# Kernel optimization log

Measured on AMD Instinct MI355X. Metric: run time of the kernel, lower is better.

## Reference

```python
import jax, jax.numpy as jnp
import numpy as np

NUM_HEADS = 4
NUM_GROUPS = 8
EPS = 1e-5


def setup_inputs() -> dict:
    key = jax.random.key(0)
    ks = jax.random.split(key, 4)
    b, c, h, w = 16, 512, 32, 32
    x = jax.random.normal(ks[0], (b, c, h, w), dtype=jnp.float32)
    gamma = jnp.ones((c,), dtype=jnp.float32)
    beta = jnp.zeros((c,), dtype=jnp.float32)
    # conv1d kernel-size-1 weights expressed as [out, in] matrices
    w_qkv = jax.random.normal(ks[1], (3 * c, c), dtype=jnp.float32) * (1.0 / np.sqrt(c))
    b_qkv = jnp.zeros((3 * c,), dtype=jnp.float32)
    w_proj = jax.random.normal(ks[2], (c, c), dtype=jnp.float32) * (1.0 / np.sqrt(c))
    b_proj = jnp.zeros((c,), dtype=jnp.float32)
    return {"x": x, "gamma": gamma, "beta": beta, "w_qkv": w_qkv,
            "b_qkv": b_qkv, "w_proj": w_proj, "b_proj": b_proj}


def group_norm(x, gamma, beta):
    # x: [b, c, h, w]; normalize per (group) over (c/g, h, w)
    b, c, h, w = x.shape
    xg = x.reshape(b, NUM_GROUPS, c // NUM_GROUPS, h, w)
    mean = xg.mean(axis=(2, 3, 4), keepdims=True)
    var = xg.var(axis=(2, 3, 4), keepdims=True)
    xn = ((xg - mean) * jax.lax.rsqrt(var + EPS)).reshape(b, c, h, w)
    return xn * gamma[None, :, None, None] + beta[None, :, None, None]


def reference(x, gamma, beta, w_qkv, b_qkv, w_proj, b_proj):
    b, c, h, w = x.shape
    L = h * w
    hd = c // NUM_HEADS  # head_dim
    x_in = x
    xn = group_norm(x, gamma, beta).reshape(b, c, L)
    # 1x1 conv == matmul over channel dim: [b, 3c, L]
    qkv = jnp.einsum('oc,bcl->bol', w_qkv, xn) + b_qkv[None, :, None]
    q, k, v = jnp.split(qkv, 3, axis=1)  # each [b, c, L]
    q = q.reshape(b, NUM_HEADS, hd, L)
    k = k.reshape(b, NUM_HEADS, hd, L)
    v = v.reshape(b, NUM_HEADS, hd, L)
    scale = hd ** (-0.5)
    attn = jnp.einsum('bhdl,bhdm->bhlm', q * scale, k)  # [b,h,L,L]
    attn = jax.nn.softmax(attn, axis=-1)
    out = jnp.einsum('bhlm,bhdm->bhdl', attn, v).reshape(b, c, L)
    out = jnp.einsum('oc,bcl->bol', w_proj, out) + b_proj[None, :, None]
    return x_in + out.reshape(b, c, h, w)
```

## Files before the change

### kernel.cpp

```cpp
#include <hip/hip_runtime.h>
#include <hip/hip_bf16.h>

typedef __hip_bfloat16 bf16;
typedef __attribute__((ext_vector_type(8))) short short8;
typedef __attribute__((ext_vector_type(4))) float f32x4;
typedef __attribute__((ext_vector_type(16))) float f32x16;

__device__ __forceinline__ float b2f(bf16 v) { return __bfloat162float(v); }
__device__ __forceinline__ bf16  f2b(float v) { return __float2bfloat16(v); }

__device__ __forceinline__ unsigned cvt_pk_bf16(float lo, float hi) {
    unsigned r;
    asm("v_cvt_pk_bf16_f32 %0, %1, %2" : "=v"(r) : "v"(lo), "v"(hi));
    return r;
}

__global__ __launch_bounds__(256) void pre_kernel(
    const float* __restrict__ wq, const float* __restrict__ wp,
    bf16* __restrict__ wqb, bf16* __restrict__ wpb,
    const float* __restrict__ x,
    float* __restrict__ partS, float* __restrict__ partQ)
{
    const int bid = blockIdx.x;
    const int t = threadIdx.x;
    if (bid < 1024) {
        int ch = bid * 256 + t;
        float4 v;
        bf16* dst;
        if (ch < 196608) {
            v = ((const float4*)wq)[ch];
            dst = wqb + ch * 4;
        } else {
            int c2 = ch - 196608;
            v = ((const float4*)wp)[c2];
            dst = wpb + c2 * 4;
        }
        bf16 o[4] = {f2b(v.x), f2b(v.y), f2b(v.z), f2b(v.w)};
        *(uint2*)dst = *(const uint2*)o;
        return;
    }
    const int pb = bid - 1024;
    const size_t base = (size_t)pb * 16384;

    float sum = 0.f, ssq = 0.f;
    const float4* x4 = (const float4*)(x + base);
    for (int i = t; i < 4096; i += 256) {
        float4 v = x4[i];
        sum += v.x + v.y + v.z + v.w;
        ssq += v.x * v.x + v.y * v.y + v.z * v.z + v.w * v.w;
    }
    #pragma unroll
    for (int off = 32; off > 0; off >>= 1) {
        sum += __shfl_down(sum, off);
        ssq += __shfl_down(ssq, off);
    }
    __shared__ float red[8];
    const int wid = t >> 6, lane = t & 63;
    if (lane == 0) { red[wid] = sum; red[4 + wid] = ssq; }
    __syncthreads();
    if (t == 0) {
        partS[pb] = red[0] + red[1] + red[2] + red[3];
        partQ[pb] = red[4] + red[5] + red[6] + red[7];
    }
}

__global__ __launch_bounds__(256) void gn_apply_t_kernel(
    const float* __restrict__ x,
    const float* __restrict__ partS, const float* __restrict__ partQ,
    const float* __restrict__ gamma, const float* __restrict__ beta,
    bf16* __restrict__ Xt)
{
    const int lt = blockIdx.x, ct = blockIdx.y, b = blockIdx.z;
    const int l0 = lt * 64, c0 = ct * 64;
    const int t = threadIdx.x;
    __shared__ float Ls[64][65];

    const int bg = b * 8 + ct;
    float s = partS[bg * 4] + partS[bg * 4 + 1] + partS[bg * 4 + 2] + partS[bg * 4 + 3];
    float q = partQ[bg * 4] + partQ[bg * 4 + 1] + partQ[bg * 4 + 2] + partQ[bg * 4 + 3];
    float mean = s * (1.f / 65536.f);
    float var  = q * (1.f / 65536.f) - mean * mean;
    float rstd = rsqrtf(var + 1e-5f);

    const float* xb = x + ((size_t)b * 512 + c0) * 1024 + l0;
    for (int i = t; i < 1024; i += 256) {
        int cc = i >> 4, lc = (i & 15) * 4;
        float4 v = *(const float4*)(xb + (size_t)cc * 1024 + lc);
        float sc = rstd * gamma[c0 + cc];
        float sh = beta[c0 + cc] - mean * sc;
        Ls[cc][lc]     = v.x * sc + sh;
        Ls[cc][lc + 1] = v.y * sc + sh;
        Ls[cc][lc + 2] = v.z * sc + sh;
        Ls[cc][lc + 3] = v.w * sc + sh;
    }
    __syncthreads();
    for (int i = t; i < 1024; i += 256) {
        int l = i >> 4, cc = (i & 15) * 4;
        bf16 o[4] = {f2b(Ls[cc][l]), f2b(Ls[cc + 1][l]),
                     f2b(Ls[cc + 2][l]), f2b(Ls[cc + 3][l])};
        *(uint2*)(Xt + ((size_t)b * 1024 + l0 + l) * 512 + c0 + cc) = *(const uint2*)o;
    }
}

__global__ __launch_bounds__(256) void mfma_qkv_kernel(
    const bf16* __restrict__ W,
    const bf16* __restrict__ Xt,
    const float* __restrict__ bias,
    bf16* __restrict__ Qt,
    bf16* __restrict__ Kt,
    bf16* __restrict__ Vb)
{
    const int n0 = blockIdx.x * 128;
    const int m0 = blockIdx.y * 128;
    const int b  = blockIdx.z;
    const int t  = threadIdx.x;
    const int w  = t >> 6, lane = t & 63;
    const int c  = lane & 15, quad = lane >> 4;
    const int w0 = w & 1, w1 = w >> 1;
    const int ak = quad * 8;

    __shared__ __align__(16) bf16 smem[18432];
    bf16* As = smem;
    bf16* Bs = smem + 9216;
    bf16* Cs = smem;

    const bf16* Ag = W + (size_t)m0 * 512;
    const bf16* Bg = Xt + ((size_t)b * 1024 + n0) * 512;

    const int srow = t >> 3, skc = (t & 7) * 8;

    short8 areg[4], breg[4];
    #pragma unroll
    for (int p = 0; p < 4; p++) {
        int row = srow + p * 32;
        areg[p] = *(const short8*)(Ag + (size_t)row * 512 + skc);
        breg[p] = *(const short8*)(Bg + (size_t)row * 512 + skc);
    }

    f32x4 acc[4][4];
    #pragma unroll
    for (int i = 0; i < 4; i++)
        #pragma unroll
        for (int j = 0; j < 4; j++)
            #pragma unroll
            for (int r = 0; r < 4; r++) acc[i][j][r] = 0.f;

    for (int k0 = 0; k0 < 512; k0 += 64) {
        __syncthreads();
        #pragma unroll
        for (int p = 0; p < 4; p++) {
            int row = srow + p * 32;
            *(short8*)&As[row * 72 + skc] = areg[p];
            *(short8*)&Bs[row * 72 + skc] = breg[p];
        }
        __syncthreads();
        {
            int k1 = (k0 + 64) & 511;
            #pragma unroll
            for (int p = 0; p < 4; p++) {
                int row = srow + p * 32;
                areg[p] = *(const short8*)(Ag + (size_t)row * 512 + k1 + skc);
                breg[p] = *(const short8*)(Bg + (size_t)row * 512 + k1 + skc);
            }
        }
        #pragma unroll
        for (int kk = 0; kk < 2; kk++) {
            short8 af[4], bf[4];
            #pragma unroll
            for (int jm = 0; jm < 4; jm++)
                af[jm] = *(const short8*)&As[(w0 * 64 + jm * 16 + c) * 72 + kk * 32 + ak];
            #pragma unroll
            for (int jn = 0; jn < 4; jn++)
                bf[jn] = *(const short8*)&Bs[(w1 * 64 + jn * 16 + c) * 72 + kk * 32 + ak];
            #pragma unroll
            for (int jm = 0; jm < 4; jm++)
                #pragma unroll
                for (int jn = 0; jn < 4; jn++)
                    acc[jm][jn] = __builtin_amdgcn_mfma_f32_16x16x32_bf16(
                        af[jm], bf[jn], acc[jm][jn], 0, 0, 0);
        }
    }

    __syncthreads();
    const int cls = m0 >> 9;
    if (cls < 2) {
        #pragma unroll
        for (int jm = 0; jm < 4; jm++) {
            #pragma unroll
            for (int jn = 0; jn < 4; jn++) {
                bf16 o4[4];
                #pragma unroll
                for (int r = 0; r < 4; r++) {
                    int orow = w0 * 64 + jm * 16 + quad * 4 + r;
                    o4[r] = f2b(acc[jm][jn][r] + bias[m0 + orow]);
                }
                *(uint2*)&Cs[(size_t)(w1 * 64 + jn * 16 + c) * 136
                             + w0 * 64 + jm * 16 + quad * 4] = *(const uint2*)o4;
            }
        }
        __syncthreads();
        const int head = (m0 >> 7) & 3;
        bf16* Db = (cls == 0 ? Qt : Kt)
                   + (((size_t)(b * 4 + head)) * 1024 + n0) * 128;
        for (int i = t; i < 2048; i += 256) {
            int row = i >> 4, ch = (i & 15) * 8;
            *(short8*)(Db + (size_t)row * 128 + ch) = *(const short8*)&Cs[row * 136 + ch];
        }
    } else {
        #pragma unroll
        for (int jm = 0; jm < 4; jm++) {
            #pragma unroll
            for (int r = 0; r < 4; r++) {
                int orow = w0 * 64 + jm * 16 + quad * 4 + r;
                float bs = bias[m0 + orow];
                #pragma unroll
                for (int jn = 0; jn < 4; jn++)
                    Cs[orow * 136 + w1 * 64 + jn * 16 + c] = f2b(acc[jm][jn][r] + bs);
            }
        }
        __syncthreads();
        bf16* Cb = Vb + ((size_t)b * 512 + (m0 - 1024)) * 1024 + n0;
        for (int i = t; i < 2048; i += 256) {
            int row = i >> 4, ch = (i & 15) * 8;
            *(short8*)(Cb + (size_t)row * 1024 + ch) = *(const short8*)&Cs[row * 136 + ch];
        }
    }
}

#define HD 128
#define QT 256
#define MT 64

__global__ __launch_bounds__(512, 2) void attn_mfma_kernel(
    const bf16* __restrict__ Qt,
    const bf16* __restrict__ Kt,
    const bf16* __restrict__ Vb,
    bf16* __restrict__ out)
{
    const int bh = blockIdx.x;
    const int qt = blockIdx.y;
    const int b = bh >> 2, h = bh & 3;
    const int t = threadIdx.x;
    const int w = t >> 6, lane = t & 63;
    const int wrow = lane & 31;
    const int blk  = lane >> 5;
    const int l0 = qt * QT;

    __shared__ __align__(16) bf16 smem[34816];

    const int qrow = w * 32 + wrow;
    const bf16* Qr = Qt + (((size_t)(b * 4 + h)) * 1024 + l0 + qrow) * 128;
    short8 aq[8];
    #pragma unroll
    for (int kt = 0; kt < 8; kt++)
        aq[kt] = *(const short8*)(Qr + kt * 16 + blk * 8);

    const bf16* Kb = Kt + (((size_t)(b * 4 + h)) * 1024) * 128;
    const bf16* Vg = Vb + ((size_t)(b * 512 + h * HD)) * 1024;

    bf16* Ks = smem;
    bf16* Vs = smem + 8704;

    short8 kreg[2], vreg[2];
    #pragma unroll
    for (int p = 0; p < 2; p++) {
        int i = t + p * 512;
        kreg[p] = *(const short8*)(Kb + (size_t)(i >> 4) * 128 + (i & 15) * 8);
        vreg[p] = *(const short8*)(Vg + (size_t)(i >> 3) * 1024 + (i & 7) * 8);
    }

    f32x16 acc_o[4];
    #pragma unroll
    for (int n = 0; n < 4; n++)
        #pragma unroll
        for (int r = 0; r < 16; r++) acc_o[n][r] = 0.f;

    float psl4[4] = {0.f, 0.f, 0.f, 0.f};

    const float kSc = 0.08838834764831845f * 1.4426950408889634f;
    const float kSh = 6.0f * 1.4426950408889634f;

    for (int mt = 0; mt < 1024 / MT; mt++) {
        __syncthreads();
        #pragma unroll
        for (int p = 0; p < 2; p++) {
            int i = t + p * 512;
            int m = i >> 4;
            int mrow = (m & 51) | ((m & 4) << 1) | ((m & 8) >> 1);
            *(short8*)&Ks[mrow * 136 + (i & 15) * 8] = kreg[p];
            *(short8*)&Vs[(i >> 3) * 72 + (i & 7) * 8]  = vreg[p];
        }
        __syncthreads();

        {
            int m0n = (mt < 15) ? (mt + 1) * MT : 0;
            #pragma unroll
            for (int p = 0; p < 2; p++) {
                int i = t + p * 512;
                kreg[p] = *(const short8*)(Kb + (size_t)(m0n + (i >> 4)) * 128 + (i & 15) * 8);
                vreg[p] = *(const short8*)(Vg + (size_t)(i >> 3) * 1024 + m0n + (i & 7) * 8);
            }
        }

        f32x16 accs[2];
        #pragma unroll
        for (int n = 0; n < 2; n++)
            #pragma unroll
            for (int r = 0; r < 16; r++) accs[n][r] = 0.f;
        __builtin_amdgcn_s_setprio(1);
        #pragma unroll
        for (int kt = 0; kt < 8; kt++) {
            #pragma unroll
            for (int nt = 0; nt < 2; nt++) {
                short8 afr = *(const short8*)&Ks[(nt * 32 + wrow) * 136 + kt * 16 + blk * 8];
                accs[nt] = __builtin_amdgcn_mfma_f32_32x32x16_bf16(afr, aq[kt], accs[nt], 0, 0, 0);
            }
        }
        __builtin_amdgcn_s_setprio(0);

        unsigned pw[2][8];
        #pragma unroll
        for (int nt = 0; nt < 2; nt++) {
            float pv[16];
            #pragma unroll
            for (int r = 0; r < 16; r++)
                pv[r] = exp2f(accs[nt][r] * kSc - kSh);
            #pragma unroll
            for (int r = 0; r < 16; r++) psl4[r & 3] += pv[r];
            #pragma unroll
            for (int wd = 0; wd < 8; wd++)
                pw[nt][wd] = cvt_pk_bf16(pv[2 * wd], pv[2 * wd + 1]);
        }

        __builtin_amdgcn_s_setprio(1);
        #pragma unroll
        for (int kt2 = 0; kt2 < 4; kt2++) {
            union { short8 s; unsigned u[4]; } pa;
            #pragma unroll
            for (int wd = 0; wd < 4; wd++)
                pa.u[wd] = pw[kt2 >> 1][(kt2 & 1) * 4 + wd];
            #pragma unroll
            for (int nt2 = 0; nt2 < 4; nt2++) {
                short8 bv = *(const short8*)&Vs[(nt2 * 32 + wrow) * 72 + kt2 * 16 + blk * 8];
                acc_o[nt2] = __builtin_amdgcn_mfma_f32_32x32x16_bf16(pa.s, bv, acc_o[nt2], 0, 0, 0);
            }
        }
        __builtin_amdgcn_s_setprio(0);
    }

    float psl = (psl4[0] + psl4[1]) + (psl4[2] + psl4[3]);
    float tot = psl + __shfl_xor(psl, 32);
    float inv[16];
    #pragma unroll
    for (int r = 0; r < 16; r++) {
        int q = (r & 3) + 8 * (r >> 2) + 4 * blk;
        inv[r] = __builtin_amdgcn_rcpf(__shfl(tot, q | (lane & 32)));
    }

    __syncthreads();
    bf16* Os = smem;
    #pragma unroll
    for (int nt2 = 0; nt2 < 4; nt2++)
        #pragma unroll
        for (int r = 0; r < 16; r++) {
            int row = w * 32 + (r & 3) + 8 * (r >> 2) + 4 * blk;
            Os[row * 136 + nt2 * 32 + wrow] = f2b(acc_o[nt2][r] * inv[r]);
        }
    __syncthreads();
    bf16* Ob = out + ((size_t)b * 1024 + l0) * 512 + h * HD;
    for (int i = t; i < 4096; i += 512) {
        int row = i >> 4, ch = (i & 15) * 8;
        *(short8*)(Ob + (size_t)row * 512 + ch) = *(const short8*)&Os[row * 136 + ch];
    }
}

__global__ __launch_bounds__(256) void mfma_proj_kernel(
    const bf16* __restrict__ W,
    const bf16* __restrict__ Xt,
    const float* __restrict__ bias,
    const float* __restrict__ res,
    float* __restrict__ C)
{
    const int n0 = blockIdx.x * 128;
    const int m0 = blockIdx.y * 128;
    const int b  = blockIdx.z;
    const int t  = threadIdx.x;
    const int w  = t >> 6, lane = t & 63;
    const int c  = lane & 15, quad = lane >> 4;
    const int w0 = w & 1, w1 = w >> 1;
    const int ak = quad * 8;

    __shared__ __align__(16) bf16 smem[18432];
    bf16* As = smem;
    bf16* Bs = smem + 9216;
    bf16* Cs = smem;

    const bf16* Ag = W + (size_t)m0 * 512;
    const bf16* Bg = Xt + ((size_t)b * 1024 + n0) * 512;

    const int srow = t >> 3, skc = (t & 7) * 8;

    short8 areg[4], breg[4];
    #pragma unroll
    for (int p = 0; p < 4; p++) {
        int row = srow + p * 32;
        areg[p] = *(const short8*)(Ag + (size_t)row * 512 + skc);
        breg[p] = *(const short8*)(Bg + (size_t)row * 512 + skc);
    }

    f32x4 acc[4][4];
    #pragma unroll
    for (int i = 0; i < 4; i++)
        #pragma unroll
        for (int j = 0; j < 4; j++)
            #pragma unroll
            for (int r = 0; r < 4; r++) acc[i][j][r] = 0.f;

    for (int k0 = 0; k0 < 512; k0 += 64) {
        __syncthreads();
        #pragma unroll
        for (int p = 0; p < 4; p++) {
            int row = srow + p * 32;
            *(short8*)&As[row * 72 + skc] = areg[p];
            *(short8*)&Bs[row * 72 + skc] = breg[p];
        }
        __syncthreads();
        {
            int k1 = (k0 + 64) & 511;
            #pragma unroll
            for (int p = 0; p < 4; p++) {
                int row = srow + p * 32;
                areg[p] = *(const short8*)(Ag + (size_t)row * 512 + k1 + skc);
                breg[p] = *(const short8*)(Bg + (size_t)row * 512 + k1 + skc);
            }
        }
        #pragma unroll
        for (int kk = 0; kk < 2; kk++) {
            short8 af[4], bf[4];
            #pragma unroll
            for (int jm = 0; jm < 4; jm++)
                af[jm] = *(const short8*)&As[(w0 * 64 + jm * 16 + c) * 72 + kk * 32 + ak];
            #pragma unroll
            for (int jn = 0; jn < 4; jn++)
                bf[jn] = *(const short8*)&Bs[(w1 * 64 + jn * 16 + c) * 72 + kk * 32 + ak];
            #pragma unroll
            for (int jm = 0; jm < 4; jm++)
                #pragma unroll
                for (int jn = 0; jn < 4; jn++)
                    acc[jm][jn] = __builtin_amdgcn_mfma_f32_16x16x32_bf16(
                        af[jm], bf[jn], acc[jm][jn], 0, 0, 0);
        }
    }

    __syncthreads();
    #pragma unroll
    for (int jm = 0; jm < 4; jm++) {
        #pragma unroll
        for (int r = 0; r < 4; r++) {
            int orow = w0 * 64 + jm * 16 + quad * 4 + r;
            float bs = bias[m0 + orow];
            #pragma unroll
            for (int jn = 0; jn < 4; jn++)
                Cs[orow * 136 + w1 * 64 + jn * 16 + c] = f2b(acc[jm][jn][r] + bs);
        }
    }
    __syncthreads();
    const float* Rb = res + ((size_t)b * 512 + m0) * 1024 + n0;
    float* Cb = C + ((size_t)b * 512 + m0) * 1024 + n0;
    for (int i = t; i < 4096; i += 256) {
        int row = i >> 5, ch = (i & 31) * 4;
        float4 rv = *(const float4*)(Rb + (size_t)row * 1024 + ch);
        float4 ov;
        ov.x = b2f(Cs[row * 136 + ch + 0]) + rv.x;
        ov.y = b2f(Cs[row * 136 + ch + 1]) + rv.y;
        ov.z = b2f(Cs[row * 136 + ch + 2]) + rv.z;
        ov.w = b2f(Cs[row * 136 + ch + 3]) + rv.w;
        *(float4*)(Cb + (size_t)row * 1024 + ch) = ov;
    }
}

extern "C" void kernel_launch(void* const* d_in, const int* in_sizes, int n_in,
                              void* d_out, int out_size, void* d_ws, size_t ws_size,
                              hipStream_t stream)
{
    const float* x      = (const float*)d_in[0];
    const float* gamma  = (const float*)d_in[1];
    const float* beta   = (const float*)d_in[2];
    const float* w_qkv  = (const float*)d_in[3];
    const float* b_qkv  = (const float*)d_in[4];
    const float* w_proj = (const float*)d_in[5];
    const float* b_proj = (const float*)d_in[6];
    float* out = (float*)d_out;

    char* ws = (char*)d_ws;
    bf16*  wqb    = (bf16*)(ws + 65536);
    bf16*  wpb    = (bf16*)(ws + 65536 + 1572864);
    char*  big    = ws + 65536 + 2097152;
    bf16*  Xt     = (bf16*)(big);
    bf16*  Qt     = (bf16*)(big + (size_t)16777216);
    bf16*  Kt     = (bf16*)(big + (size_t)2 * 16777216);
    bf16*  Vb     = (bf16*)(big + (size_t)3 * 16777216);
    float* partS  = (float*)(big + (size_t)4 * 16777216);
    float* partQ  = partS + 512;
    bf16*  attn_t = Xt;

    hipLaunchKernelGGL(pre_kernel, dim3(1536), dim3(256), 0, stream,
                       w_qkv, w_proj, wqb, wpb, x, partS, partQ);
    hipLaunchKernelGGL(gn_apply_t_kernel, dim3(16, 8, 16), dim3(256), 0, stream,
                       x, partS, partQ, gamma, beta, Xt);
    hipLaunchKernelGGL(mfma_qkv_kernel, dim3(8, 12, 16), dim3(256), 0, stream,
                       wqb, Xt, b_qkv, Qt, Kt, Vb);
    hipLaunchKernelGGL(attn_mfma_kernel, dim3(64, 4), dim3(512), 0, stream,
                       Qt, Kt, Vb, attn_t);
    hipLaunchKernelGGL(mfma_proj_kernel, dim3(8, 4, 16), dim3(256), 0, stream,
                       wpb, attn_t, b_proj, x, out);
}
```

Before: 216.3 us.

## Stage GEMM tiles directly to LDS with double-buffered global_load_lds

The QKV and projection GEMM main loops now use global_load_lds to copy A and B tiles straight from global memory into LDS. This replaces the old path of loading into registers and then writing to a padded LDS buffer. The K-step drops from 64 to 32 and the loop keeps two LDS buffers, so the next tile can be fetched while the current one feeds MFMAs, with one barrier per step. The aim is to save VGPRs and ds_write instructions. In exchange, the unpadded 32-element row layout may cause LDS bank conflicts, there are twice as many barriers, and correctness depends on the compiler waiting for the async LDS loads before each barrier.

```diff
diff --git a/kernel.cpp b/kernel.cpp
--- a/kernel.cpp
+++ b/kernel.cpp
@@ -13,6 +13,21 @@
     unsigned r;
     asm("v_cvt_pk_bf16_f32 %0, %1, %2" : "=v"(r) : "v"(lo), "v"(hi));
     return r;
+}
+
+__device__ __forceinline__ void stage_tile_gld(
+    const bf16* __restrict__ gbase, bf16* lbuf, int t)
+{
+    const int lane = t & 63, w = t >> 6;
+    #pragma unroll
+    for (int p = 0; p < 2; p++) {
+        int row = p * 64 + w * 16 + (lane >> 2);
+        __builtin_amdgcn_global_load_lds(
+            (const __attribute__((address_space(1))) void*)
+                (gbase + (size_t)row * 512 + (lane & 3) * 8),
+            (__attribute__((address_space(3))) void*)(lbuf + p * 2048 + w * 512),
+            16, 0, 0);
+    }
 }
 
 __global__ __launch_bounds__(256) void pre_kernel(
@@ -119,24 +134,12 @@
     const int w0 = w & 1, w1 = w >> 1;
     const int ak = quad * 8;
 
-    __shared__ __align__(16) bf16 smem[18432];
-    bf16* As = smem;
-    bf16* Bs = smem + 9216;
+    __shared__ __align__(16) bf16 smem[17408];
     bf16* Cs = smem;
 
     const bf16* Ag = W + (size_t)m0 * 512;
     const bf16* Bg = Xt + ((size_t)b * 1024 + n0) * 512;
 
-    const int srow = t >> 3, skc = (t & 7) * 8;
-
-    short8 areg[4], breg[4];
-    #pragma unroll
-    for (int p = 0; p < 4; p++) {
-        int row = srow + p * 32;
-        areg[p] = *(const short8*)(Ag + (size_t)row * 512 + skc);
-        breg[p] = *(const short8*)(Bg + (size_t)row * 512 + skc);
-    }
-
     f32x4 acc[4][4];
     #pragma unroll
     for (int i = 0; i < 4; i++)
@@ -145,40 +148,33 @@
             #pragma unroll
             for (int r = 0; r < 4; r++) acc[i][j][r] = 0.f;
 
-    for (int k0 = 0; k0 < 512; k0 += 64) {
-        __syncthreads();
-        #pragma unroll
-        for (int p = 0; p < 4; p++) {
-            int row = srow + p * 32;
-            *(short8*)&As[row * 72 + skc] = areg[p];
-            *(short8*)&Bs[row * 72 + skc] = breg[p];
-        }
-        __syncthreads();
-        {
-            int k1 = (k0 + 64) & 511;
-            #pragma unroll
-            for (int p = 0; p < 4; p++) {
-                int row = srow + p * 32;
-                areg[p] = *(const short8*)(Ag + (size_t)row * 512 + k1 + skc);
-                breg[p] = *(const short8*)(Bg + (size_t)row * 512 + k1 + skc);
-            }
-        }
-        #pragma unroll
-        for (int kk = 0; kk < 2; kk++) {
-            short8 af[4], bf[4];
-            #pragma unroll
-            for (int jm = 0; jm < 4; jm++)
-                af[jm] = *(const short8*)&As[(w0 * 64 + jm * 16 + c) * 72 + kk * 32 + ak];
+    stage_tile_gld(Ag, smem, t);
+    stage_tile_gld(Bg, smem + 4096, t);
+
+    int cur = 0;
+    for (int k0 = 0; k0 < 512; k0 += 32) {
+        __syncthreads();
+        if (k0 + 32 < 512) {
+            bf16* nb = smem + (cur ^ 1) * 8192;
+            stage_tile_gld(Ag + k0 + 32, nb, t);
+            stage_tile_gld(Bg + k0 + 32, nb + 4096, t);
+        }
+        const bf16* As = smem + cur * 8192;
+        const bf16* Bs = As + 4096;
+        short8 af[4], bfr[4];
+        #pragma unroll
+        for (int jm = 0; jm < 4; jm++)
+            af[jm] = *(const short8*)&As[(w0 * 64 + jm * 16 + c) * 32 + ak];
+        #pragma unroll
+        for (int jn = 0; jn < 4; jn++)
+            bfr[jn] = *(const short8*)&Bs[(w1 * 64 + jn * 16 + c) * 32 + ak];
+        #pragma unroll
+        for (int jm = 0; jm < 4; jm++)
             #pragma unroll
             for (int jn = 0; jn < 4; jn++)
-                bf[jn] = *(const short8*)&Bs[(w1 * 64 + jn * 16 + c) * 72 + kk * 32 + ak];
-            #pragma unroll
-            for (int jm = 0; jm < 4; jm++)
-                #pragma unroll
-                for (int jn = 0; jn < 4; jn++)
-                    acc[jm][jn] = __builtin_amdgcn_mfma_f32_16x16x32_bf16(
-                        af[jm], bf[jn], acc[jm][jn], 0, 0, 0);
-        }
+                acc[jm][jn] = __builtin_amdgcn_mfma_f32_16x16x32_bf16(
+                    af[jm], bfr[jn], acc[jm][jn], 0, 0, 0);
+        cur ^= 1;
     }
 
     __syncthreads();
@@ -390,24 +386,12 @@
     const int w0 = w & 1, w1 = w >> 1;
     const int ak = quad * 8;
 
-    __shared__ __align__(16) bf16 smem[18432];
-    bf16* As = smem;
-    bf16* Bs = smem + 9216;
+    __shared__ __align__(16) bf16 smem[17408];
     bf16* Cs = smem;
 
     const bf16* Ag = W + (size_t)m0 * 512;
     const bf16* Bg = Xt + ((size_t)b * 1024 + n0) * 512;
 
-    const int srow = t >> 3, skc = (t & 7) * 8;
-
-    short8 areg[4], breg[4];
-    #pragma unroll
-    for (int p = 0; p < 4; p++) {
-        int row = srow + p * 32;
-        areg[p] = *(const short8*)(Ag + (size_t)row * 512 + skc);
-        breg[p] = *(const short8*)(Bg + (size_t)row * 512 + skc);
-    }
-
     f32x4 acc[4][4];
     #pragma unroll
     for (int i = 0; i < 4; i++)
@@ -416,40 +400,33 @@
             #pragma unroll
             for (int r = 0; r < 4; r++) acc[i][j][r] = 0.f;
 
-    for (int k0 = 0; k0 < 512; k0 += 64) {
-        __syncthreads();
-        #pragma unroll
-        for (int p = 0; p < 4; p++) {
-            int row = srow + p * 32;
-            *(short8*)&As[row * 72 + skc] = areg[p];
-            *(short8*)&Bs[row * 72 + skc] = breg[p];
-        }
-        __syncthreads();
-        {
-            int k1 = (k0 + 64) & 511;
-            #pragma unroll
-            for (int p = 0; p < 4; p++) {
-                int row = srow + p * 32;
-                areg[p] = *(const short8*)(Ag + (size_t)row * 512 + k1 + skc);
-                breg[p] = *(const short8*)(Bg + (size_t)row * 512 + k1 + skc);
-            }
-        }
-        #pragma unroll
-        for (int kk = 0; kk < 2; kk++) {
-            short8 af[4], bf[4];
-            #pragma unroll
-            for (int jm = 0; jm < 4; jm++)
-                af[jm] = *(const short8*)&As[(w0 * 64 + jm * 16 + c) * 72 + kk * 32 + ak];
+    stage_tile_gld(Ag, smem, t);
+    stage_tile_gld(Bg, smem + 4096, t);
+
+    int cur = 0;
+    for (int k0 = 0; k0 < 512; k0 += 32) {
+        __syncthreads();
+        if (k0 + 32 < 512) {
+            bf16* nb = smem + (cur ^ 1) * 8192;
+            stage_tile_gld(Ag + k0 + 32, nb, t);
+            stage_tile_gld(Bg + k0 + 32, nb + 4096, t);
+        }
+        const bf16* As = smem + cur * 8192;
+        const bf16* Bs = As + 4096;
+        short8 af[4], bfr[4];
+        #pragma unroll
+        for (int jm = 0; jm < 4; jm++)
+            af[jm] = *(const short8*)&As[(w0 * 64 + jm * 16 + c) * 32 + ak];
+        #pragma unroll
+        for (int jn = 0; jn < 4; jn++)
+            bfr[jn] = *(const short8*)&Bs[(w1 * 64 + jn * 16 + c) * 32 + ak];
+        #pragma unroll
+        for (int jm = 0; jm < 4; jm++)
             #pragma unroll
             for (int jn = 0; jn < 4; jn++)
-                bf[jn] = *(const short8*)&Bs[(w1 * 64 + jn * 16 + c) * 72 + kk * 32 + ak];
-            #pragma unroll
-            for (int jm = 0; jm < 4; jm++)
-                #pragma unroll
-                for (int jn = 0; jn < 4; jn++)
-                    acc[jm][jn] = __builtin_amdgcn_mfma_f32_16x16x32_bf16(
-                        af[jm], bf[jn], acc[jm][jn], 0, 0, 0);
-        }
+                acc[jm][jn] = __builtin_amdgcn_mfma_f32_16x16x32_bf16(
+                    af[jm], bfr[jn], acc[jm][jn], 0, 0, 0);
+        cur ^= 1;
     }
 
     __syncthreads();
```

Measured after the change: 209.9 us. -3.0%, faster.
